# Kernel tuning notes

Measured on AMD Instinct MI355X. Metric: run time of the kernel, lower is better.

Reference implementation:

```python
import jax, jax.numpy as jnp
import numpy as np

H = 16   # num_heads
HD = 64  # head_dim
D = 1024 # hidden_dim
SCALE = 1.0 / (HD ** 0.5)

def setup_inputs() -> dict:
    key = jax.random.key(0)
    ks = jax.random.split(key, 12)
    B, S = 4, 2048
    init = lambda k, shape: jax.random.normal(k, shape, jnp.float32) * 0.02
    return {
        "query": jax.random.normal(ks[0], (B, S, D), jnp.float32),
        "key": jax.random.normal(ks[1], (B, S, D), jnp.float32),
        "value": jax.random.normal(ks[2], (B, S, D), jnp.float32),
        "attention_mask": jax.random.randint(ks[3], (B, S, S), 0, 2).astype(jnp.bool_),
        "Wq": init(ks[4], (D, H * HD)), "bq": jnp.zeros((H * HD,), jnp.float32),
        "Wk": init(ks[5], (D, H * HD)), "bk": jnp.zeros((H * HD,), jnp.float32),
        "Wv": init(ks[6], (D, H * HD)), "bv": jnp.zeros((H * HD,), jnp.float32),
        "Wo": init(ks[7], (H * HD, D)), "bo": jnp.zeros((D,), jnp.float32),
    }

def reference(query, key, value, attention_mask, Wq, bq, Wk, bk, Wv, bv, Wo, bo):
    B, S, _ = query.shape
    # QKV projections -> [B, H, S, HD]
    def split_heads(x):
        return x.reshape(B, -1, H, HD).transpose(0, 2, 1, 3)
    Q = split_heads(query @ Wq + bq)
    K = split_heads(key @ Wk + bk)
    V = split_heads(value @ Wv + bv)
    # scores: [B, H, S, S]
    scores = jnp.einsum('bhqd,bhkd->bhqk', Q, K) * SCALE
    scores = jnp.where(attention_mask[:, None, :, :], -1e9, scores)
    attn = jax.nn.softmax(scores, axis=-1)
    # dropout is identity in eval mode
    context = jnp.einsum('bhqk,bhkd->bhqd', attn, V)
    context = context.transpose(0, 2, 1, 3).reshape(B, -1, H * HD)
    outputs = context @ Wo + bo
    return (outputs, attn)
```

## Files before the change

### kernel.cpp

```cpp
#include <hip/hip_runtime.h>
#include <hip/hip_bf16.h>

#define S_    2048
#define D_    1024
#define H_    16
#define HD_   64
#define NB_   4

using bf16x8 = __attribute__((ext_vector_type(8))) short;
using f32x4  = __attribute__((ext_vector_type(4))) float;

static __device__ __forceinline__ short f2bf(float f) {
  unsigned u = __builtin_bit_cast(unsigned, f);
  u += 0x7fffu + ((u >> 16) & 1u);
  return (short)(u >> 16);
}
static __device__ __forceinline__ unsigned pk2(float a, float b) {
  return (unsigned)(unsigned short)f2bf(a) | ((unsigned)(unsigned short)f2bf(b) << 16);
}

static __device__ __forceinline__ void gld16(const short* g, short* l) {
  __builtin_amdgcn_global_load_lds(
      (const __attribute__((address_space(1))) void*)g,
      (__attribute__((address_space(3))) void*)l, 16, 0, 0);
}

__global__ __launch_bounds__(256) void cast_kernel(const float* __restrict__ src,
                                                   short* __restrict__ dst, int n8) {
  int i = blockIdx.x * 256 + threadIdx.x;
  if (i >= n8) return;
  f32x4 a = reinterpret_cast<const f32x4*>(src)[2 * i];
  f32x4 b = reinterpret_cast<const f32x4*>(src)[2 * i + 1];
  bf16x8 o;
  o[0] = f2bf(a[0]); o[1] = f2bf(a[1]); o[2] = f2bf(a[2]); o[3] = f2bf(a[3]);
  o[4] = f2bf(b[0]); o[5] = f2bf(b[1]); o[6] = f2bf(b[2]); o[7] = f2bf(b[3]);
  reinterpret_cast<bf16x8*>(dst)[i] = o;
}

__global__ __launch_bounds__(256) void pack_mask(const int* __restrict__ mask,
                                                 unsigned long long* __restrict__ mp) {
  int i = blockIdx.x * 256 + threadIdx.x;
  unsigned long long bits = __ballot(mask[i] != 0);
  if ((threadIdx.x & 63) == 0) {
    int k = i & 2047;
    int q = (i >> 11) & 2047;
    int b = i >> 22;
    mp[((size_t)(b * 32 + (k >> 6))) * 2048 + q] = bits;
  }
}

__global__ __launch_bounds__(256) void transpose_cast_kernel(const float* __restrict__ W,
                                                             short* __restrict__ Wt) {
  __shared__ float tile[32][33];
  int tx = threadIdx.x, ty = threadIdx.y;
  int bx = blockIdx.x * 32, by = blockIdx.y * 32;
#pragma unroll
  for (int i = 0; i < 4; ++i) {
    int k = ty + 8 * i;
    tile[k][tx] = W[(size_t)(by + k) * D_ + bx + tx];
  }
  __syncthreads();
#pragma unroll
  for (int i = 0; i < 4; ++i) {
    int n = ty + 8 * i;
    Wt[(size_t)(bx + n) * D_ + by + tx] = f2bf(tile[tx][n]);
  }
}

template <int MODE>
__global__ __launch_bounds__(256) void proj_gemm(const short* __restrict__ A,
                                                 const short* __restrict__ Bt,
                                                 const float* __restrict__ bias,
                                                 void* __restrict__ outp, float oscale) {
  __shared__ short As[128 * 64];
  __shared__ short Bs[128 * 64];
  const int t = threadIdx.x;
  const int w = t >> 6, l = t & 63, lr = l & 15, lg = l >> 4;
  const int rb = blockIdx.x, cb = blockIdx.y;
  const int wr = w >> 1, wc = w & 1;
  const f32x4 fz = {0.f, 0.f, 0.f, 0.f};
  f32x4 acc[4][4];
#pragma unroll
  for (int mi = 0; mi < 4; ++mi)
#pragma unroll
    for (int ni = 0; ni < 4; ++ni) acc[mi][ni] = fz;

  const int sr = l >> 3;
  const int sd = (l & 7) ^ sr;
  const short* Ag = A + ((size_t)(rb * 128 + w * 8 + sr)) * D_ + sd * 8;
  const short* Bg = Bt + ((size_t)(cb * 128 + w * 8 + sr)) * D_ + sd * 8;

  for (int k0 = 0; k0 < D_; k0 += 64) {
    __syncthreads();
#pragma unroll
    for (int i = 0; i < 4; ++i) {
      gld16(Ag + (size_t)(32 * i) * D_ + k0, &As[(4 * i + w) * 512]);
      gld16(Bg + (size_t)(32 * i) * D_ + k0, &Bs[(4 * i + w) * 512]);
    }
    __syncthreads();
#pragma unroll
    for (int kk = 0; kk < 2; ++kk) {
      bf16x8 af[4], bfr[4];
#pragma unroll
      for (int mi = 0; mi < 4; ++mi) {
        int r = wr * 64 + mi * 16 + lr;
        af[mi] = *reinterpret_cast<bf16x8*>(&As[r * 64 + (((4 * kk + lg) ^ (lr & 7)) * 8)]);
      }
#pragma unroll
      for (int ni = 0; ni < 4; ++ni) {
        int r = wc * 64 + ni * 16 + lr;
        bfr[ni] = *reinterpret_cast<bf16x8*>(&Bs[r * 64 + (((4 * kk + lg) ^ (lr & 7)) * 8)]);
      }
#pragma unroll
      for (int mi = 0; mi < 4; ++mi)
#pragma unroll
        for (int ni = 0; ni < 4; ++ni)
          acc[mi][ni] = __builtin_amdgcn_mfma_f32_16x16x32_bf16(af[mi], bfr[ni], acc[mi][ni], 0, 0, 0);
    }
  }

#pragma unroll
  for (int mi = 0; mi < 4; ++mi) {
#pragma unroll
    for (int ni = 0; ni < 4; ++ni) {
#pragma unroll
      for (int j = 0; j < 4; ++j) {
        int rr = rb * 128 + wr * 64 + mi * 16 + 4 * lg + j;
        int cc = cb * 128 + wc * 64 + ni * 16 + lr;
        float v = acc[mi][ni][j] + bias[cc];
        int b = rr >> 11, s = rr & 2047, h = cc >> 6, d = cc & 63;
        if (MODE == 0) {
          ((short*)outp)[(((size_t)(b * H_ + h)) * S_ + s) * HD_ + d] = f2bf(v * oscale);
        } else if (MODE == 1) {
          ((short*)outp)[(((size_t)(b * H_ + h)) * HD_ + d) * S_ + s] = f2bf(v);
        } else {
          ((float*)outp)[(size_t)rr * D_ + cc] = v;
        }
      }
    }
  }
}

__global__ __launch_bounds__(256, 2) void attn_kernel(const short* __restrict__ Q,
                                                      const short* __restrict__ K,
                                                      const short* __restrict__ Vt,
                                                      const unsigned long long* __restrict__ mT,
                                                      float* __restrict__ attn_out,
                                                      short* __restrict__ ctx) {
  __shared__ __attribute__((aligned(16))) char smem[34816];
  short* Ps  = (short*)smem;
  float* mlb = (float*)(smem + 9216);
  float* c4  = (float*)smem;

  const int tid = threadIdx.x;
  const int w = tid >> 6, l = tid & 63, lr = l & 15, lg = l >> 4;
  const int bid = blockIdx.x;
  const int swz = (bid & 7) * 256 + (bid >> 3);
  const int qt = swz & 31, bh = swz >> 5;
  const int b = bh >> 4, h = bh & 15;

  const short* Qg = Q + ((size_t)bh * S_ + qt * 64) * HD_;
  const short* Kg = K + (size_t)bh * S_ * HD_;
  const short* Vg = Vt + (size_t)bh * HD_ * S_;
  const f32x4 fz = {0.f, 0.f, 0.f, 0.f};

  bf16x8 qf[4][2];
#pragma unroll
  for (int qa = 0; qa < 4; ++qa)
#pragma unroll
    for (int c = 0; c < 2; ++c)
      qf[qa][c] = *reinterpret_cast<const bf16x8*>(&Qg[(size_t)(16 * qa + lr) * HD_ + 32 * c + 8 * lg]);

  float ls[4] = {0.f, 0.f, 0.f, 0.f};

#pragma unroll 1
  for (int t8 = 0; t8 < 8; ++t8) {
    const int kt = t8 * 4 + w;
    const short* kb = Kg + (size_t)kt * 64 * HD_;
    bf16x8 kf[4][2];
#pragma unroll
    for (int nf = 0; nf < 4; ++nf)
#pragma unroll
      for (int c = 0; c < 2; ++c)
        kf[nf][c] = *reinterpret_cast<const bf16x8*>(&kb[(size_t)(16 * nf + lr) * HD_ + 32 * c + 8 * lg]);
    unsigned long long mw[4];
#pragma unroll
    for (int qa = 0; qa < 4; ++qa)
      mw[qa] = mT[(size_t)(b * 32 + kt) * S_ + qt * 64 + 16 * qa + lr];
    __builtin_amdgcn_sched_barrier(0);

#pragma unroll
    for (int qa = 0; qa < 4; ++qa) {
      f32x4 sc[4];
      __builtin_amdgcn_s_setprio(1);
#pragma unroll
      for (int nf = 0; nf < 4; ++nf) {
        f32x4 a = fz;
        a = __builtin_amdgcn_mfma_f32_16x16x32_bf16(kf[nf][0], qf[qa][0], a, 0, 0, 0);
        a = __builtin_amdgcn_mfma_f32_16x16x32_bf16(kf[nf][1], qf[qa][1], a, 0, 0, 0);
        sc[nf] = a;
      }
      __builtin_amdgcn_s_setprio(0);
      float acc = 0.0f;
#pragma unroll
      for (int nf = 0; nf < 4; ++nf) {
        unsigned nib = (unsigned)(mw[qa] >> (16 * nf + 4 * lg)) & 0xFu;
        float e[4];
#pragma unroll
        for (int j = 0; j < 4; ++j) {
          float v = __builtin_amdgcn_exp2f(sc[nf][j]);
          e[j] = ((nib >> j) & 1) ? 0.0f : v;
        }
        acc += (e[0] + e[1]) + (e[2] + e[3]);
      }
      ls[qa] += acc;
    }
  }
#pragma unroll
  for (int off = 16; off < 64; off <<= 1)
#pragma unroll
    for (int qa = 0; qa < 4; ++qa) ls[qa] += __shfl_xor(ls[qa], off, 64);
  if (lg == 0) {
#pragma unroll
    for (int qa = 0; qa < 4; ++qa) mlb[(w * 4 + qa) * 16 + lr] = ls[qa];
  }
  __syncthreads();
  float rl[4];
#pragma unroll
  for (int qa = 0; qa < 4; ++qa) {
    float lt = (mlb[(0 * 4 + qa) * 16 + lr] + mlb[(1 * 4 + qa) * 16 + lr]) +
               (mlb[(2 * 4 + qa) * 16 + lr] + mlb[(3 * 4 + qa) * 16 + lr]);
    rl[qa] = 1.0f / lt;
  }

  f32x4 ctxa[4][4];
#pragma unroll
  for (int qa = 0; qa < 4; ++qa)
#pragma unroll
    for (int df = 0; df < 4; ++df) ctxa[qa][df] = fz;
  short* Pw = Ps + w * 16 * 72;

#pragma unroll 1
  for (int t8 = 0; t8 < 8; ++t8) {
    const int kt = t8 * 4 + w;
    const short* kb = Kg + (size_t)kt * 64 * HD_;
    bf16x8 kf[4][2], vf[4][2];
#pragma unroll
    for (int nf = 0; nf < 4; ++nf)
#pragma unroll
      for (int c = 0; c < 2; ++c)
        kf[nf][c] = *reinterpret_cast<const bf16x8*>(&kb[(size_t)(16 * nf + lr) * HD_ + 32 * c + 8 * lg]);
#pragma unroll
    for (int df = 0; df < 4; ++df)
#pragma unroll
      for (int c = 0; c < 2; ++c)
        vf[df][c] = *reinterpret_cast<const bf16x8*>(&Vg[(size_t)(16 * df + lr) * S_ + kt * 64 + 32 * c + 8 * lg]);
    unsigned long long mw[4];
#pragma unroll
    for (int qa = 0; qa < 4; ++qa)
      mw[qa] = mT[(size_t)(b * 32 + kt) * S_ + qt * 64 + 16 * qa + lr];
    __builtin_amdgcn_sched_barrier(0);

#pragma unroll
    for (int qa = 0; qa < 4; ++qa) {
      f32x4 sc[4];
      __builtin_amdgcn_s_setprio(1);
#pragma unroll
      for (int nf = 0; nf < 4; ++nf) {
        f32x4 a = fz;
        a = __builtin_amdgcn_mfma_f32_16x16x32_bf16(kf[nf][0], qf[qa][0], a, 0, 0, 0);
        a = __builtin_amdgcn_mfma_f32_16x16x32_bf16(kf[nf][1], qf[qa][1], a, 0, 0, 0);
        sc[nf] = a;
      }
      __builtin_amdgcn_s_setprio(0);
      float* arow = attn_out + ((size_t)bh * S_ + (qt * 64 + 16 * qa + lr)) * S_ + kt * 64;
      uint2 U[4];
#pragma unroll
      for (int nf = 0; nf < 4; ++nf) {
        unsigned nib = (unsigned)(mw[qa] >> (16 * nf + 4 * lg)) & 0xFu;
        f32x4 pv;
#pragma unroll
        for (int j = 0; j < 4; ++j) {
          float e = __builtin_amdgcn_exp2f(sc[nf][j]) * rl[qa];
          pv[j] = ((nib >> j) & 1) ? 0.0f : e;
        }
        __builtin_nontemporal_store(pv, (f32x4*)(arow + 16 * nf + 4 * lg));
        U[nf].x = pk2(pv[0], pv[1]);
        U[nf].y = pk2(pv[2], pv[3]);
      }
#pragma unroll
      for (int nf = 0; nf < 4; ++nf)
        *reinterpret_cast<uint2*>(&Pw[lr * 72 + 16 * nf + 4 * lg]) = U[nf];
      __builtin_amdgcn_sched_barrier(0);
      asm volatile("s_waitcnt lgkmcnt(0)");
      __builtin_amdgcn_sched_barrier(0);
      bf16x8 pa0 = *reinterpret_cast<bf16x8*>(&Pw[lr * 72 + 8 * lg]);
      bf16x8 pa1 = *reinterpret_cast<bf16x8*>(&Pw[lr * 72 + 32 + 8 * lg]);
      __builtin_amdgcn_s_setprio(1);
#pragma unroll
      for (int df = 0; df < 4; ++df) {
        ctxa[qa][df] = __builtin_amdgcn_mfma_f32_16x16x32_bf16(pa0, vf[df][0], ctxa[qa][df], 0, 0, 0);
        ctxa[qa][df] = __builtin_amdgcn_mfma_f32_16x16x32_bf16(pa1, vf[df][1], ctxa[qa][df], 0, 0, 0);
      }
      __builtin_amdgcn_s_setprio(0);
    }
  }

  __syncthreads();
#pragma unroll
  for (int r = 0; r < 2; ++r) {
    if (r) __syncthreads();
#pragma unroll
    for (int qa = 0; qa < 4; ++qa)
#pragma unroll
      for (int dh = 0; dh < 2; ++dh) {
        int dl = 16 * dh + lr;
        *reinterpret_cast<f32x4*>(&c4[(size_t)(w * 32 + dl) * 68 + 16 * qa + 4 * lg]) =
            ctxa[qa][2 * r + dh];
      }
    __syncthreads();
    int q = tid & 63, d0 = (tid >> 6) * 8;
    float vs[8];
#pragma unroll
    for (int i = 0; i < 8; ++i) {
      int dl = d0 + i;
      vs[i] = (c4[(0 * 32 + dl) * 68 + q] + c4[(1 * 32 + dl) * 68 + q]) +
              (c4[(2 * 32 + dl) * 68 + q] + c4[(3 * 32 + dl) * 68 + q]);
    }
    bf16x8 o;
#pragma unroll
    for (int i = 0; i < 8; ++i) o[i] = f2bf(vs[i]);
    *reinterpret_cast<bf16x8*>(&ctx[((size_t)b * S_ + qt * 64 + q) * D_ + h * 64 + 32 * r + d0]) = o;
  }
}

extern "C" void kernel_launch(void* const* d_in, const int* in_sizes, int n_in,
                              void* d_out, int out_size, void* d_ws, size_t ws_size,
                              hipStream_t stream) {
  const float* query = (const float*)d_in[0];
  const float* key   = (const float*)d_in[1];
  const float* value = (const float*)d_in[2];
  const int*   mask  = (const int*)d_in[3];
  const float* Wq = (const float*)d_in[4];
  const float* bq = (const float*)d_in[5];
  const float* Wk = (const float*)d_in[6];
  const float* bk = (const float*)d_in[7];
  const float* Wv = (const float*)d_in[8];
  const float* bv = (const float*)d_in[9];
  const float* Wo = (const float*)d_in[10];
  const float* bo = (const float*)d_in[11];

  char* ws = (char*)d_ws;
  const size_t BIG = 16777216;
  short* Xbuf  = (short*)(ws);
  short* Qbuf  = (short*)(ws + BIG);
  short* Kbuf  = (short*)(ws + 2 * BIG);
  short* Vtbuf = (short*)(ws + 3 * BIG);
  short* Wqt   = (short*)(ws + 4 * BIG);
  short* Wkt   = (short*)(ws + 4 * BIG + 2097152);
  short* Wvt   = (short*)(ws + 4 * BIG + 2 * 2097152);
  short* Wot   = (short*)(ws + 4 * BIG + 3 * 2097152);
  unsigned long long* maskp = (unsigned long long*)(ws + 4 * BIG + 4 * 2097152);
  short* ctx   = Xbuf;

  float* out0 = (float*)d_out;
  float* attn_out = out0 + (size_t)NB_ * S_ * D_;

  pack_mask<<<(NB_ * S_ * S_) / 256, 256, 0, stream>>>(mask, maskp);

  dim3 tcb(32, 8), tcg(32, 32);
  transpose_cast_kernel<<<tcg, tcb, 0, stream>>>(Wq, Wqt);
  transpose_cast_kernel<<<tcg, tcb, 0, stream>>>(Wk, Wkt);
  transpose_cast_kernel<<<tcg, tcb, 0, stream>>>(Wv, Wvt);
  transpose_cast_kernel<<<tcg, tcb, 0, stream>>>(Wo, Wot);

  const int n8 = (NB_ * S_ * D_) / 8;
  dim3 gemm_g(64, 8);
  const float QSCALE = 0.125f * 1.4426950408889634f;

  cast_kernel<<<n8 / 256, 256, 0, stream>>>(query, Xbuf, n8);
  proj_gemm<0><<<gemm_g, 256, 0, stream>>>(Xbuf, Wqt, bq, Qbuf, QSCALE);
  cast_kernel<<<n8 / 256, 256, 0, stream>>>(key, Xbuf, n8);
  proj_gemm<0><<<gemm_g, 256, 0, stream>>>(Xbuf, Wkt, bk, Kbuf, 1.0f);
  cast_kernel<<<n8 / 256, 256, 0, stream>>>(value, Xbuf, n8);
  proj_gemm<1><<<gemm_g, 256, 0, stream>>>(Xbuf, Wvt, bv, Vtbuf, 1.0f);

  attn_kernel<<<2048, 256, 0, stream>>>(Qbuf, Kbuf, Vtbuf, maskp, attn_out, ctx);

  proj_gemm<2><<<gemm_g, 256, 0, stream>>>(ctx, Wot, bo, out0, 1.0f);
}
```

Measured before the change: 476.1 us.

## Split attention into row-sum pass and output pass with double-buffered K loads

Splits the fused attention kernel into two launches. The first computes the masked softmax row denominators, stores their reciprocals to a workspace buffer, and runs at higher occupancy. The second reads those reciprocals and produces the attention probabilities and context. Both passes now double-buffer the K fragments and mask words across key tiles so loads overlap with MFMA work. This costs an extra launch, a re-read of Q, and more register pressure from the duplicate fragment buffers.

```diff
diff --git a/kernel.cpp b/kernel.cpp
--- a/kernel.cpp
+++ b/kernel.cpp
@@ -141,16 +141,114 @@
   }
 }
 
-__global__ __launch_bounds__(256, 2) void attn_kernel(const short* __restrict__ Q,
-                                                      const short* __restrict__ K,
-                                                      const short* __restrict__ Vt,
-                                                      const unsigned long long* __restrict__ mT,
-                                                      float* __restrict__ attn_out,
-                                                      short* __restrict__ ctx) {
+__global__ __launch_bounds__(256, 3) void attn_pass1(const short* __restrict__ Q,
+                                                     const short* __restrict__ K,
+                                                     const unsigned long long* __restrict__ mT,
+                                                     float* __restrict__ rlbuf) {
+  __shared__ float mlb[4 * 4 * 16];
+  const int tid = threadIdx.x;
+  const int w = tid >> 6, l = tid & 63, lr = l & 15, lg = l >> 4;
+  const int bid = blockIdx.x;
+  const int swz = (bid & 7) * 256 + (bid >> 3);
+  const int qt = swz & 31, bh = swz >> 5;
+  const int b = bh >> 4;
+
+  const short* Qg = Q + ((size_t)bh * S_ + qt * 64) * HD_;
+  const short* Kg = K + (size_t)bh * S_ * HD_;
+  const f32x4 fz = {0.f, 0.f, 0.f, 0.f};
+
+  bf16x8 qf[4][2];
+#pragma unroll
+  for (int qa = 0; qa < 4; ++qa)
+#pragma unroll
+    for (int c = 0; c < 2; ++c)
+      qf[qa][c] = *reinterpret_cast<const bf16x8*>(&Qg[(size_t)(16 * qa + lr) * HD_ + 32 * c + 8 * lg]);
+
+  float ls[4] = {0.f, 0.f, 0.f, 0.f};
+  bf16x8 kfA[4][2], kfB[4][2];
+  unsigned long long mwA[4], mwB[4];
+
+  auto LOADK = [&](bf16x8 (&kf)[4][2], unsigned long long (&mw)[4], int i) {
+    const int kt = 4 * i + w;
+    const short* kb = Kg + (size_t)kt * 64 * HD_;
+#pragma unroll
+    for (int nf = 0; nf < 4; ++nf)
+#pragma unroll
+      for (int c = 0; c < 2; ++c)
+        kf[nf][c] = *reinterpret_cast<const bf16x8*>(&kb[(size_t)(16 * nf + lr) * HD_ + 32 * c + 8 * lg]);
+#pragma unroll
+    for (int qa = 0; qa < 4; ++qa)
+      mw[qa] = mT[(size_t)(b * 32 + kt) * S_ + qt * 64 + 16 * qa + lr];
+  };
+  auto STEP = [&](bf16x8 (&kf)[4][2], unsigned long long (&mw)[4]) {
+#pragma unroll
+    for (int qa = 0; qa < 4; ++qa) {
+      f32x4 sc[4];
+      __builtin_amdgcn_s_setprio(1);
+#pragma unroll
+      for (int nf = 0; nf < 4; ++nf) {
+        f32x4 a = fz;
+        a = __builtin_amdgcn_mfma_f32_16x16x32_bf16(kf[nf][0], qf[qa][0], a, 0, 0, 0);
+        a = __builtin_amdgcn_mfma_f32_16x16x32_bf16(kf[nf][1], qf[qa][1], a, 0, 0, 0);
+        sc[nf] = a;
+      }
+      __builtin_amdgcn_s_setprio(0);
+      float acc = 0.0f;
+#pragma unroll
+      for (int nf = 0; nf < 4; ++nf) {
+        unsigned nib = (unsigned)(mw[qa] >> (16 * nf + 4 * lg)) & 0xFu;
+        float e[4];
+#pragma unroll
+        for (int j = 0; j < 4; ++j) {
+          float v = __builtin_amdgcn_exp2f(sc[nf][j]);
+          e[j] = ((nib >> j) & 1) ? 0.0f : v;
+        }
+        acc += (e[0] + e[1]) + (e[2] + e[3]);
+      }
+      ls[qa] += acc;
+    }
+  };
+
+  LOADK(kfA, mwA, 0);
+#pragma unroll 1
+  for (int tp = 0; tp < 4; ++tp) {
+    LOADK(kfB, mwB, 2 * tp + 1);
+    __builtin_amdgcn_sched_barrier(0);
+    STEP(kfA, mwA);
+    if (tp < 3) LOADK(kfA, mwA, 2 * tp + 2);
+    __builtin_amdgcn_sched_barrier(0);
+    STEP(kfB, mwB);
+  }
+
+#pragma unroll
+  for (int off = 16; off < 64; off <<= 1)
+#pragma unroll
+    for (int qa = 0; qa < 4; ++qa) ls[qa] += __shfl_xor(ls[qa], off, 64);
+  if (lg == 0) {
+#pragma unroll
+    for (int qa = 0; qa < 4; ++qa) mlb[(w * 4 + qa) * 16 + lr] = ls[qa];
+  }
+  __syncthreads();
+  if (w == 0 && lg == 0) {
+#pragma unroll
+    for (int qa = 0; qa < 4; ++qa) {
+      float lt = (mlb[(0 * 4 + qa) * 16 + lr] + mlb[(1 * 4 + qa) * 16 + lr]) +
+                 (mlb[(2 * 4 + qa) * 16 + lr] + mlb[(3 * 4 + qa) * 16 + lr]);
+      rlbuf[(size_t)bh * S_ + qt * 64 + 16 * qa + lr] = 1.0f / lt;
+    }
+  }
+}
+
+__global__ __launch_bounds__(256, 2) void attn_pass2(const short* __restrict__ Q,
+                                                     const short* __restrict__ K,
+                                                     const short* __restrict__ Vt,
+                                                     const unsigned long long* __restrict__ mT,
+                                                     const float* __restrict__ rlbuf,
+                                                     float* __restrict__ attn_out,
+                                                     short* __restrict__ ctx) {
   __shared__ __attribute__((aligned(16))) char smem[34816];
-  short* Ps  = (short*)smem;
-  float* mlb = (float*)(smem + 9216);
-  float* c4  = (float*)smem;
+  short* Ps = (short*)smem;
+  float* c4 = (float*)smem;
 
   const int tid = threadIdx.x;
   const int w = tid >> 6, l = tid & 63, lr = l & 15, lg = l >> 4;
@@ -171,96 +269,43 @@
     for (int c = 0; c < 2; ++c)
       qf[qa][c] = *reinterpret_cast<const bf16x8*>(&Qg[(size_t)(16 * qa + lr) * HD_ + 32 * c + 8 * lg]);
 
-  float ls[4] = {0.f, 0.f, 0.f, 0.f};
-
-#pragma unroll 1
-  for (int t8 = 0; t8 < 8; ++t8) {
-    const int kt = t8 * 4 + w;
+  float rl[4];
+#pragma unroll
+  for (int qa = 0; qa < 4; ++qa)
+    rl[qa] = rlbuf[(size_t)bh * S_ + qt * 64 + 16 * qa + lr];
+
+  f32x4 ctxa[4][4];
+#pragma unroll
+  for (int qa = 0; qa < 4; ++qa)
+#pragma unroll
+    for (int df = 0; df < 4; ++df) ctxa[qa][df] = fz;
+  short* Pw = Ps + w * 16 * 72;
+
+  bf16x8 kfA[4][2], kfB[4][2];
+  unsigned long long mwA[4], mwB[4];
+
+  auto LOADK = [&](bf16x8 (&kf)[4][2], unsigned long long (&mw)[4], int i) {
+    const int kt = 4 * i + w;
     const short* kb = Kg + (size_t)kt * 64 * HD_;
-    bf16x8 kf[4][2];
 #pragma unroll
     for (int nf = 0; nf < 4; ++nf)
 #pragma unroll
       for (int c = 0; c < 2; ++c)
         kf[nf][c] = *reinterpret_cast<const bf16x8*>(&kb[(size_t)(16 * nf + lr) * HD_ + 32 * c + 8 * lg]);
-    unsigned long long mw[4];
 #pragma unroll
     for (int qa = 0; qa < 4; ++qa)
       mw[qa] = mT[(size_t)(b * 32 + kt) * S_ + qt * 64 + 16 * qa + lr];
-    __builtin_amdgcn_sched_barrier(0);
-
-#pragma unroll
-    for (int qa = 0; qa < 4; ++qa) {
-      f32x4 sc[4];
-      __builtin_amdgcn_s_setprio(1);
-#pragma unroll
-      for (int nf = 0; nf < 4; ++nf) {
-        f32x4 a = fz;
-        a = __builtin_amdgcn_mfma_f32_16x16x32_bf16(kf[nf][0], qf[qa][0], a, 0, 0, 0);
-        a = __builtin_amdgcn_mfma_f32_16x16x32_bf16(kf[nf][1], qf[qa][1], a, 0, 0, 0);
-        sc[nf] = a;
-      }
-      __builtin_amdgcn_s_setprio(0);
-      float acc = 0.0f;
-#pragma unroll
-      for (int nf = 0; nf < 4; ++nf) {
-        unsigned nib = (unsigned)(mw[qa] >> (16 * nf + 4 * lg)) & 0xFu;
-        float e[4];
-#pragma unroll
-        for (int j = 0; j < 4; ++j) {
-          float v = __builtin_amdgcn_exp2f(sc[nf][j]);
-          e[j] = ((nib >> j) & 1) ? 0.0f : v;
-        }
-        acc += (e[0] + e[1]) + (e[2] + e[3]);
-      }
-      ls[qa] += acc;
-    }
-  }
-#pragma unroll
-  for (int off = 16; off < 64; off <<= 1)
-#pragma unroll
-    for (int qa = 0; qa < 4; ++qa) ls[qa] += __shfl_xor(ls[qa], off, 64);
-  if (lg == 0) {
-#pragma unroll
-    for (int qa = 0; qa < 4; ++qa) mlb[(w * 4 + qa) * 16 + lr] = ls[qa];
-  }
-  __syncthreads();
-  float rl[4];
-#pragma unroll
-  for (int qa = 0; qa < 4; ++qa) {
-    float lt = (mlb[(0 * 4 + qa) * 16 + lr] + mlb[(1 * 4 + qa) * 16 + lr]) +
-               (mlb[(2 * 4 + qa) * 16 + lr] + mlb[(3 * 4 + qa) * 16 + lr]);
-    rl[qa] = 1.0f / lt;
-  }
-
-  f32x4 ctxa[4][4];
-#pragma unroll
-  for (int qa = 0; qa < 4; ++qa)
-#pragma unroll
-    for (int df = 0; df < 4; ++df) ctxa[qa][df] = fz;
-  short* Pw = Ps + w * 16 * 72;
-
-#pragma unroll 1
-  for (int t8 = 0; t8 < 8; ++t8) {
-    const int kt = t8 * 4 + w;
-    const short* kb = Kg + (size_t)kt * 64 * HD_;
-    bf16x8 kf[4][2], vf[4][2];
-#pragma unroll
-    for (int nf = 0; nf < 4; ++nf)
-#pragma unroll
-      for (int c = 0; c < 2; ++c)
-        kf[nf][c] = *reinterpret_cast<const bf16x8*>(&kb[(size_t)(16 * nf + lr) * HD_ + 32 * c + 8 * lg]);
+  };
+
+  auto STEP = [&](bf16x8 (&kf)[4][2], unsigned long long (&mw)[4], int i) {
+    const int kt = 4 * i + w;
+    bf16x8 vf[4][2];
 #pragma unroll
     for (int df = 0; df < 4; ++df)
 #pragma unroll
       for (int c = 0; c < 2; ++c)
         vf[df][c] = *reinterpret_cast<const bf16x8*>(&Vg[(size_t)(16 * df + lr) * S_ + kt * 64 + 32 * c + 8 * lg]);
-    unsigned long long mw[4];
-#pragma unroll
-    for (int qa = 0; qa < 4; ++qa)
-      mw[qa] = mT[(size_t)(b * 32 + kt) * S_ + qt * 64 + 16 * qa + lr];
     __builtin_amdgcn_sched_barrier(0);
-
 #pragma unroll
     for (int qa = 0; qa < 4; ++qa) {
       f32x4 sc[4];
@@ -304,6 +349,17 @@
       }
       __builtin_amdgcn_s_setprio(0);
     }
+  };
+
+  LOADK(kfA, mwA, 0);
+#pragma unroll 1
+  for (int tp = 0; tp < 4; ++tp) {
+    LOADK(kfB, mwB, 2 * tp + 1);
+    __builtin_amdgcn_sched_barrier(0);
+    STEP(kfA, mwA, 2 * tp);
+    if (tp < 3) LOADK(kfA, mwA, 2 * tp + 2);
+    __builtin_amdgcn_sched_barrier(0);
+    STEP(kfB, mwB, 2 * tp + 1);
   }
 
   __syncthreads();
@@ -361,6 +417,7 @@
   short* Wvt   = (short*)(ws + 4 * BIG + 2 * 2097152);
   short* Wot   = (short*)(ws + 4 * BIG + 3 * 2097152);
   unsigned long long* maskp = (unsigned long long*)(ws + 4 * BIG + 4 * 2097152);
+  float* rlbuf = (float*)(ws + 4 * BIG + 4 * 2097152 + 2097152);
   short* ctx   = Xbuf;
 
   float* out0 = (float*)d_out;
@@ -385,7 +442,8 @@
   cast_kernel<<<n8 / 256, 256, 0, stream>>>(value, Xbuf, n8);
   proj_gemm<1><<<gemm_g, 256, 0, stream>>>(Xbuf, Wvt, bv, Vtbuf, 1.0f);
 
-  attn_kernel<<<2048, 256, 0, stream>>>(Qbuf, Kbuf, Vtbuf, maskp, attn_out, ctx);
+  attn_pass1<<<2048, 256, 0, stream>>>(Qbuf, Kbuf, maskp, rlbuf);
+  attn_pass2<<<2048, 256, 0, stream>>>(Qbuf, Kbuf, Vtbuf, maskp, rlbuf, attn_out, ctx);
 
   proj_gemm<2><<<gemm_g, 256, 0, stream>>>(ctx, Wot, bo, out0, 1.0f);
 }
```

Result: slower. 774.5 us (+62.7%).
